# Optimization experiments

Measured on AMD Instinct MI355X. Metric: run time of the kernel, lower is better.

The kernel has to match this reference:

```python
import jax, jax.numpy as jnp
import numpy as np

B, S, E, H, MAXLEN = 2, 2048, 1024, 16, 2048


def _level_indices(seq_len: int, base: int = 2) -> np.ndarray:
    """Vectorized version of get_level_index_weak over the full (target, source) grid.
    indices[t, s] = min(level, 2) for s < t, else 0. Runs in O(log S) passes."""
    tt = np.broadcast_to(np.arange(seq_len)[:, None], (seq_len, seq_len)).astype(np.int64).copy()
    ss = np.broadcast_to(np.arange(seq_len)[None, :], (seq_len, seq_len)).astype(np.int64).copy()
    res = np.zeros((seq_len, seq_len), np.int64)
    done = ~(ss < tt)  # only source < target positions get a level; rest stay 0
    while not done.all():
        l = np.floor(np.log2(np.maximum(tt, 1).astype(np.float64))).astype(np.int64)
        v = (np.int64(1) << l)
        hit = (~done) & (ss < v)
        res[hit] = l[hit] + 1
        done |= hit
        step = ~done
        tt[step] -= v[step]
        ss[step] -= v[step]
    return np.minimum(res, 2).astype(np.int32)


def setup_inputs() -> dict:
    key = jax.random.key(0)
    ks = jax.random.split(key, 10)
    sc = 0.02
    return {
        "x": jax.random.normal(ks[0], (B, S, E), dtype=jnp.float32),
        "attention_mask": jax.random.randint(ks[1], (B, S), 0, 2, dtype=jnp.int32),
        "level_indices": jnp.asarray(_level_indices(S, 2)),
        "Wq": jax.random.normal(ks[2], (E, E), dtype=jnp.float32) * sc,
        "bq": jnp.zeros((E,), jnp.float32),
        "Wk": jax.random.normal(ks[3], (E, E), dtype=jnp.float32) * sc,
        "bk": jnp.zeros((E,), jnp.float32),
        "Wv": jax.random.normal(ks[4], (E, E), dtype=jnp.float32) * sc,
        "bv": jnp.zeros((E,), jnp.float32),
        "hier": jax.random.normal(ks[5], (MAXLEN, H, 3), dtype=jnp.float32),
        "Wo": jax.random.normal(ks[6], (E, E), dtype=jnp.float32) * sc,
        "bo": jnp.zeros((E,), jnp.float32),
    }


def reference(x, attention_mask, level_indices, Wq, bq, Wk, bk, Wv, bv, hier, Wo, bo):
    b, s, e = x.shape
    h = hier.shape[1]
    dh = e // h
    # q/k are computed by the original module but never used; kept for fidelity (zero grads).
    q = x @ Wq.T + bq
    k = x @ Wk.T + bk
    v = (x @ Wv.T + bv).reshape(b, s, h, dh).transpose(0, 2, 1, 3)  # [B,H,S,Dh]
    lev = level_indices[:s, :s]  # [S,S] int, values in {0,1,2}
    # Faithful torch.gather semantics: weights[b,h,i,j] = hier[b, h, lev[i,j]]
    w3 = hier[:b]                      # [B,H,3]
    weights = w3[:, :, lev]            # [B,H,S,S]
    decay = jnp.power(jnp.float32(0.5), lev.astype(x.dtype))  # [S,S]
    weights = weights * decay
    weights = weights / (jnp.sum(weights, axis=-1, keepdims=True) + 1e-8)
    weights = jnp.where(attention_mask[:, None, None, :] == 0, jnp.float32(0.0), weights)
    out = jnp.einsum('bhij,bhjd->bhid', weights, v)  # [B,H,S,Dh]
    out = out.transpose(0, 2, 1, 3).reshape(b, s, e)
    return out @ Wo.T + bo
```

## Files before the change

kernel.cpp:

```cpp
#include <hip/hip_runtime.h>
#include <cstdint>
#include <cstddef>

constexpr int Sn = 2048;
constexpr int En = 1024;
constexpr int Bn = 2;
constexpr int Hn = 16;
constexpr int NCH = 32;
constexpr int CHUNK = 64;

typedef __bf16 bf16x8 __attribute__((ext_vector_type(8)));
typedef float  f32x4  __attribute__((ext_vector_type(4)));

#define GLOBAL_AS(p) ((const __attribute__((address_space(1))) void*)(p))
#define LDS_AS(p)    ((__attribute__((address_space(3))) void*)(p))

__device__ __forceinline__ unsigned short f2bf(float f) {
    union { float f; uint32_t u; } v; v.f = f;
    const uint32_t u = v.u;
    return (unsigned short)((u + 0x7fffu + ((u >> 16) & 1u)) >> 16);
}
__device__ __forceinline__ float bf2f_lo(uint32_t u) {
    union { uint32_t u; float f; } v; v.u = u << 16; return v.f;
}
__device__ __forceinline__ float bf2f_hi(uint32_t u) {
    union { uint32_t u; float f; } v; v.u = u & 0xffff0000u; return v.f;
}

constexpr int XN = Bn * Sn * En;
constexpr int WN = En * En;

__global__ __launch_bounds__(256)
void cast3(const float* __restrict__ x, const float* __restrict__ Wv,
           const float* __restrict__ Wo, unsigned short* __restrict__ xb,
           unsigned short* __restrict__ Wvb, unsigned short* __restrict__ Wob)
{
    const int i = (blockIdx.x * 256 + threadIdx.x) * 4;
    const float* src; unsigned short* dst; int off;
    if (i < XN)           { src = x;  dst = xb;  off = i; }
    else if (i < XN + WN) { src = Wv; dst = Wvb; off = i - XN; }
    else                  { src = Wo; dst = Wob; off = i - XN - WN; }
    const float4 v = *(const float4*)(src + off);
    ushort4 o;
    o.x = f2bf(v.x); o.y = f2bf(v.y); o.z = f2bf(v.z); o.w = f2bf(v.w);
    *(ushort4*)(dst + off) = o;
}

template<bool APPLY_MASK, bool OUT_BF16, bool FUSE_CSUM>
__global__ __launch_bounds__(256)
void gemm_mfma(const unsigned short* __restrict__ A, const unsigned short* __restrict__ Bw,
               const float* __restrict__ bias, const int* __restrict__ mask,
               void* __restrict__ Cv, float* __restrict__ csum, int M, int N, int K)
{
    __shared__ __align__(16) unsigned short As[128 * 64];
    __shared__ __align__(16) unsigned short Bs[64 * 64];

    const int tid  = threadIdx.x;
    const int lane = tid & 63;
    const int wv   = tid >> 6;
    const int wr   = wv >> 1;
    const int wc   = wv & 1;
    const int bm   = blockIdx.y * 128;
    const int bn   = blockIdx.x * 64;
    const int m16  = lane & 15;
    const int kq   = lane >> 4;

    f32x4 acc[4][2] = {};

    const int j0 = 2 * wv, j1 = 2 * wv + 1;
    const unsigned short* gA0 = A  + (size_t)(bm + 16 * j0 + m16) * K + kq * 8;
    const unsigned short* gA1 = A  + (size_t)(bm + 16 * j1 + m16) * K + kq * 8;
    const unsigned short* gB0 = Bw + (size_t)(bn + 16 * wv + m16) * K + kq * 8;
    unsigned short* lA00 = &As[(j0 * 2 + 0) * 512];
    unsigned short* lA01 = &As[(j0 * 2 + 1) * 512];
    unsigned short* lA10 = &As[(j1 * 2 + 0) * 512];
    unsigned short* lA11 = &As[(j1 * 2 + 1) * 512];
    unsigned short* lB00 = &Bs[(wv * 2 + 0) * 512];
    unsigned short* lB01 = &Bs[(wv * 2 + 1) * 512];

    for (int k0 = 0; k0 < K; k0 += 64) {
        __syncthreads();
        __builtin_amdgcn_global_load_lds(GLOBAL_AS(gA0 + k0),      LDS_AS(lA00), 16, 0, 0);
        __builtin_amdgcn_global_load_lds(GLOBAL_AS(gA0 + k0 + 32), LDS_AS(lA01), 16, 0, 0);
        __builtin_amdgcn_global_load_lds(GLOBAL_AS(gA1 + k0),      LDS_AS(lA10), 16, 0, 0);
        __builtin_amdgcn_global_load_lds(GLOBAL_AS(gA1 + k0 + 32), LDS_AS(lA11), 16, 0, 0);
        __builtin_amdgcn_global_load_lds(GLOBAL_AS(gB0 + k0),      LDS_AS(lB00), 16, 0, 0);
        __builtin_amdgcn_global_load_lds(GLOBAL_AS(gB0 + k0 + 32), LDS_AS(lB01), 16, 0, 0);
        __syncthreads();

        bf16x8 af[4][2], bfr[2][2];
#pragma unroll
        for (int i = 0; i < 4; ++i)
#pragma unroll
            for (int kk = 0; kk < 2; ++kk)
                af[i][kk] = *(const bf16x8*)&As[((wr * 4 + i) * 2 + kk) * 512 + lane * 8];
#pragma unroll
        for (int j = 0; j < 2; ++j)
#pragma unroll
            for (int kk = 0; kk < 2; ++kk)
                bfr[j][kk] = *(const bf16x8*)&Bs[((wc * 2 + j) * 2 + kk) * 512 + lane * 8];
#pragma unroll
        for (int kk = 0; kk < 2; ++kk)
#pragma unroll
            for (int i = 0; i < 4; ++i)
#pragma unroll
                for (int j = 0; j < 2; ++j)
                    acc[i][j] = __builtin_amdgcn_mfma_f32_16x16x32_bf16(af[i][kk], bfr[j][kk], acc[i][j], 0, 0, 0);
    }

    float colsum[2] = {0.0f, 0.0f};
#pragma unroll
    for (int i = 0; i < 4; ++i) {
        const int r0 = bm + wr * 64 + i * 16 + kq * 4;
#pragma unroll
        for (int j = 0; j < 2; ++j) {
            const int c0 = bn + wc * 32 + j * 16 + m16;
            const float bcol = bias[c0];
#pragma unroll
            for (int r = 0; r < 4; ++r) {
                const int row = r0 + r;
                float val = acc[i][j][r] + bcol;
                if (APPLY_MASK) val = (mask[row] == 0) ? 0.0f : val;
                if (FUSE_CSUM) colsum[j] += val;
                if (OUT_BF16)
                    ((unsigned short*)Cv)[(size_t)row * N + c0] = f2bf(val);
                else
                    ((float*)Cv)[(size_t)row * N + c0] = val;
            }
        }
    }

    if (FUSE_CSUM) {
        const int gc = 2 * blockIdx.y + wr;
#pragma unroll
        for (int j = 0; j < 2; ++j) {
            float s = colsum[j];
            s += __shfl_xor(s, 16, 64);
            s += __shfl_xor(s, 32, 64);
            if (kq == 0)
                csum[(size_t)gc * En + bn + wc * 32 + j * 16 + m16] = s;
        }
    }
}

__global__ __launch_bounds__(256)
void chunk_scan(const float* __restrict__ csum, float* __restrict__ cscan,
                float* __restrict__ Tbuf)
{
    const int idx = blockIdx.x * 256 + threadIdx.x;
    float run = 0.0f;
    const int b = idx >> 10;
    const int e = idx & (En - 1);
    for (int c = 0; c < NCH; ++c) {
        const size_t off = ((size_t)b * NCH + c) * En + e;
        const float v = csum[off];
        cscan[off] = run;
        run += v;
    }
    Tbuf[idx] = run;
}

__global__ __launch_bounds__(256)
void combine(const unsigned short* __restrict__ vm, const float* __restrict__ cscan,
             const float* __restrict__ Tbuf, const float* __restrict__ hier,
             unsigned short* __restrict__ opre)
{
    const int ep = blockIdx.x * 256 + threadIdx.x;
    const int e = ep * 2;
    const int c = blockIdx.y;
    const int b = blockIdx.z;
    const int h = e >> 6;

    const float w0 = hier[((size_t)b * Hn + h) * 3 + 0];
    const float w1 = hier[((size_t)b * Hn + h) * 3 + 1] * 0.5f;
    const float w2 = hier[((size_t)b * Hn + h) * 3 + 2] * 0.25f;
    const float T0 = Tbuf[(size_t)b * En + e];
    const float T1 = Tbuf[(size_t)b * En + e + 1];

    const size_t co = ((size_t)b * NCH + c) * En + e;
    float run0 = cscan[co], run1 = cscan[co + 1];
    float prev0 = 0.0f, prev1 = 0.0f;
    const size_t base = ((size_t)b * Sn + c * CHUNK) * En + e;

    for (int t = 0; t < CHUNK; ++t) {
        const int i = c * CHUNK + t;
        const uint32_t u = *(const uint32_t*)(vm + base + (size_t)t * En);
        const float cur0 = bf2f_lo(u), cur1 = bf2f_hi(u);
        float num0, num1, Z;
        if (i & 1) {
            num0 = w2 * (run0 - prev0) + w1 * prev0 + w0 * (T0 - run0);
            num1 = w2 * (run1 - prev1) + w1 * prev1 + w0 * (T1 - run1);
            Z = (float)(i - 1) * w2 + w1 + (float)(Sn - i) * w0 + 1e-8f;
        } else {
            num0 = w2 * run0 + w0 * (T0 - run0);
            num1 = w2 * run1 + w0 * (T1 - run1);
            Z = (float)i * w2 + (float)(Sn - i) * w0 + 1e-8f;
        }
        const float rz = 1.0f / Z;
        const uint32_t o = (uint32_t)f2bf(num0 * rz) | ((uint32_t)f2bf(num1 * rz) << 16);
        *(uint32_t*)(opre + base + (size_t)t * En) = o;
        run0 += cur0; run1 += cur1;
        prev0 = cur0; prev1 = cur1;
    }
}

extern "C" void kernel_launch(void* const* d_in, const int* in_sizes, int n_in,
                              void* d_out, int out_size, void* d_ws, size_t ws_size,
                              hipStream_t stream)
{
    const float* x    = (const float*)d_in[0];
    const int*   mask = (const int*)d_in[1];
    const float* Wv   = (const float*)d_in[7];
    const float* bv   = (const float*)d_in[8];
    const float* hier = (const float*)d_in[9];
    const float* Wo   = (const float*)d_in[10];
    const float* bo   = (const float*)d_in[11];
    float* out = (float*)d_out;

    const int M = Bn * Sn, N = En, K = En;

    char* ws = (char*)d_ws;
    unsigned short* xb    = (unsigned short*)ws;  ws += (size_t)M * K * 2;
    unsigned short* Wvb   = (unsigned short*)ws;  ws += (size_t)N * K * 2;
    unsigned short* Wob   = (unsigned short*)ws;  ws += (size_t)N * K * 2;
    unsigned short* vmb   = (unsigned short*)ws;  ws += (size_t)M * N * 2;
    float*          csum  = (float*)ws;           ws += (size_t)Bn * NCH * En * 4;
    float*          cscan = (float*)ws;           ws += (size_t)Bn * NCH * En * 4;
    float*          Tbuf  = (float*)ws;           ws += (size_t)Bn * En * 4;
    unsigned short* opreb = (unsigned short*)ws;  ws += (size_t)M * N * 2;

    dim3 threads(256);

    cast3<<<dim3((XN + 2 * WN) / 1024), threads, 0, stream>>>(x, Wv, Wo, xb, Wvb, Wob);

    dim3 gemm_grid(N / 64, M / 128);

    gemm_mfma<true, true, true><<<gemm_grid, threads, 0, stream>>>(xb, Wvb, bv, mask, vmb, csum, M, N, K);
    chunk_scan<<<dim3((Bn * En) / 256), threads, 0, stream>>>(csum, cscan, Tbuf);
    combine<<<dim3(En / 512, NCH, Bn), threads, 0, stream>>>(vmb, cscan, Tbuf, hier, opreb);
    gemm_mfma<false, false, false><<<gemm_grid, threads, 0, stream>>>(opreb, Wob, bo, nullptr, out, nullptr, M, N, K);
}
```

Baseline: 172.3 us.

## Switch GEMMs to 128x128 split-K tiles with separate reduction kernels

Both GEMMs now use 128x128 output tiles with K split in two across blockIdx.z, writing fp32 partials to a workspace. New reduce kernels sum the partials and apply bias, mask, bf16 cast and per-chunk column sums. The chunk_scan kernel is dropped; combine recomputes the prefix and total from csum itself. This raises per-tile reuse and keeps the grid at 512 blocks, but it adds about 32 MB of fp32 partial traffic per GEMM plus two extra launches.

```diff
diff --git a/kernel.cpp b/kernel.cpp
--- a/kernel.cpp
+++ b/kernel.cpp
@@ -8,6 +8,8 @@
 constexpr int Hn = 16;
 constexpr int NCH = 32;
 constexpr int CHUNK = 64;
+constexpr int Mtot = Bn * Sn;
+constexpr int GCH = Mtot / CHUNK;
 
 typedef __bf16 bf16x8 __attribute__((ext_vector_type(8)));
 typedef float  f32x4  __attribute__((ext_vector_type(4)));
@@ -46,14 +48,12 @@
     *(ushort4*)(dst + off) = o;
 }
 
-template<bool APPLY_MASK, bool OUT_BF16, bool FUSE_CSUM>
-__global__ __launch_bounds__(256)
-void gemm_mfma(const unsigned short* __restrict__ A, const unsigned short* __restrict__ Bw,
-               const float* __restrict__ bias, const int* __restrict__ mask,
-               void* __restrict__ Cv, float* __restrict__ csum, int M, int N, int K)
+__global__ __launch_bounds__(256)
+void gemm_splitk(const unsigned short* __restrict__ A, const unsigned short* __restrict__ Bw,
+                 float* __restrict__ Part, int M, int N, int K)
 {
     __shared__ __align__(16) unsigned short As[128 * 64];
-    __shared__ __align__(16) unsigned short Bs[64 * 64];
+    __shared__ __align__(16) unsigned short Bs[128 * 64];
 
     const int tid  = threadIdx.x;
     const int lane = tid & 63;
@@ -61,24 +61,30 @@
     const int wr   = wv >> 1;
     const int wc   = wv & 1;
     const int bm   = blockIdx.y * 128;
-    const int bn   = blockIdx.x * 64;
+    const int bn   = blockIdx.x * 128;
+    const int ks   = blockIdx.z;
     const int m16  = lane & 15;
     const int kq   = lane >> 4;
 
-    f32x4 acc[4][2] = {};
-
-    const int j0 = 2 * wv, j1 = 2 * wv + 1;
-    const unsigned short* gA0 = A  + (size_t)(bm + 16 * j0 + m16) * K + kq * 8;
-    const unsigned short* gA1 = A  + (size_t)(bm + 16 * j1 + m16) * K + kq * 8;
-    const unsigned short* gB0 = Bw + (size_t)(bn + 16 * wv + m16) * K + kq * 8;
-    unsigned short* lA00 = &As[(j0 * 2 + 0) * 512];
-    unsigned short* lA01 = &As[(j0 * 2 + 1) * 512];
-    unsigned short* lA10 = &As[(j1 * 2 + 0) * 512];
-    unsigned short* lA11 = &As[(j1 * 2 + 1) * 512];
-    unsigned short* lB00 = &Bs[(wv * 2 + 0) * 512];
-    unsigned short* lB01 = &Bs[(wv * 2 + 1) * 512];
-
-    for (int k0 = 0; k0 < K; k0 += 64) {
+    const int kbase = ks * (K / 2);
+
+    f32x4 acc[4][4] = {};
+
+    const int rg0 = 2 * wv, rg1 = 2 * wv + 1;
+    const unsigned short* gA0 = A  + (size_t)(bm + 16 * rg0 + m16) * K + kbase + kq * 8;
+    const unsigned short* gA1 = A  + (size_t)(bm + 16 * rg1 + m16) * K + kbase + kq * 8;
+    const unsigned short* gB0 = Bw + (size_t)(bn + 16 * rg0 + m16) * K + kbase + kq * 8;
+    const unsigned short* gB1 = Bw + (size_t)(bn + 16 * rg1 + m16) * K + kbase + kq * 8;
+    unsigned short* lA00 = &As[(rg0 * 2 + 0) * 512];
+    unsigned short* lA01 = &As[(rg0 * 2 + 1) * 512];
+    unsigned short* lA10 = &As[(rg1 * 2 + 0) * 512];
+    unsigned short* lA11 = &As[(rg1 * 2 + 1) * 512];
+    unsigned short* lB00 = &Bs[(rg0 * 2 + 0) * 512];
+    unsigned short* lB01 = &Bs[(rg0 * 2 + 1) * 512];
+    unsigned short* lB10 = &Bs[(rg1 * 2 + 0) * 512];
+    unsigned short* lB11 = &Bs[(rg1 * 2 + 1) * 512];
+
+    for (int k0 = 0; k0 < K / 2; k0 += 64) {
         __syncthreads();
         __builtin_amdgcn_global_load_lds(GLOBAL_AS(gA0 + k0),      LDS_AS(lA00), 16, 0, 0);
         __builtin_amdgcn_global_load_lds(GLOBAL_AS(gA0 + k0 + 32), LDS_AS(lA01), 16, 0, 0);
@@ -86,84 +92,81 @@
         __builtin_amdgcn_global_load_lds(GLOBAL_AS(gA1 + k0 + 32), LDS_AS(lA11), 16, 0, 0);
         __builtin_amdgcn_global_load_lds(GLOBAL_AS(gB0 + k0),      LDS_AS(lB00), 16, 0, 0);
         __builtin_amdgcn_global_load_lds(GLOBAL_AS(gB0 + k0 + 32), LDS_AS(lB01), 16, 0, 0);
+        __builtin_amdgcn_global_load_lds(GLOBAL_AS(gB1 + k0),      LDS_AS(lB10), 16, 0, 0);
+        __builtin_amdgcn_global_load_lds(GLOBAL_AS(gB1 + k0 + 32), LDS_AS(lB11), 16, 0, 0);
         __syncthreads();
 
-        bf16x8 af[4][2], bfr[2][2];
+        bf16x8 af[4][2], bfr[4][2];
 #pragma unroll
         for (int i = 0; i < 4; ++i)
 #pragma unroll
-            for (int kk = 0; kk < 2; ++kk)
-                af[i][kk] = *(const bf16x8*)&As[((wr * 4 + i) * 2 + kk) * 512 + lane * 8];
-#pragma unroll
-        for (int j = 0; j < 2; ++j)
-#pragma unroll
-            for (int kk = 0; kk < 2; ++kk)
-                bfr[j][kk] = *(const bf16x8*)&Bs[((wc * 2 + j) * 2 + kk) * 512 + lane * 8];
-#pragma unroll
-        for (int kk = 0; kk < 2; ++kk)
+            for (int kh = 0; kh < 2; ++kh) {
+                af[i][kh]  = *(const bf16x8*)&As[(((wr * 4 + i) * 2) + kh) * 512 + lane * 8];
+                bfr[i][kh] = *(const bf16x8*)&Bs[(((wc * 4 + i) * 2) + kh) * 512 + lane * 8];
+            }
+#pragma unroll
+        for (int kh = 0; kh < 2; ++kh)
 #pragma unroll
             for (int i = 0; i < 4; ++i)
 #pragma unroll
-                for (int j = 0; j < 2; ++j)
-                    acc[i][j] = __builtin_amdgcn_mfma_f32_16x16x32_bf16(af[i][kk], bfr[j][kk], acc[i][j], 0, 0, 0);
-    }
-
-    float colsum[2] = {0.0f, 0.0f};
+                for (int j = 0; j < 4; ++j)
+                    acc[i][j] = __builtin_amdgcn_mfma_f32_16x16x32_bf16(af[i][kh], bfr[j][kh], acc[i][j], 0, 0, 0);
+    }
+
+    float* P = Part + (size_t)ks * M * N;
 #pragma unroll
     for (int i = 0; i < 4; ++i) {
         const int r0 = bm + wr * 64 + i * 16 + kq * 4;
 #pragma unroll
-        for (int j = 0; j < 2; ++j) {
-            const int c0 = bn + wc * 32 + j * 16 + m16;
-            const float bcol = bias[c0];
-#pragma unroll
-            for (int r = 0; r < 4; ++r) {
-                const int row = r0 + r;
-                float val = acc[i][j][r] + bcol;
-                if (APPLY_MASK) val = (mask[row] == 0) ? 0.0f : val;
-                if (FUSE_CSUM) colsum[j] += val;
-                if (OUT_BF16)
-                    ((unsigned short*)Cv)[(size_t)row * N + c0] = f2bf(val);
-                else
-                    ((float*)Cv)[(size_t)row * N + c0] = val;
-            }
+        for (int j = 0; j < 4; ++j) {
+            const int c0 = bn + wc * 64 + j * 16 + m16;
+#pragma unroll
+            for (int r = 0; r < 4; ++r)
+                P[(size_t)(r0 + r) * N + c0] = acc[i][j][r];
         }
     }
-
-    if (FUSE_CSUM) {
-        const int gc = 2 * blockIdx.y + wr;
-#pragma unroll
-        for (int j = 0; j < 2; ++j) {
-            float s = colsum[j];
-            s += __shfl_xor(s, 16, 64);
-            s += __shfl_xor(s, 32, 64);
-            if (kq == 0)
-                csum[(size_t)gc * En + bn + wc * 32 + j * 16 + m16] = s;
-        }
-    }
-}
-
-__global__ __launch_bounds__(256)
-void chunk_scan(const float* __restrict__ csum, float* __restrict__ cscan,
-                float* __restrict__ Tbuf)
-{
-    const int idx = blockIdx.x * 256 + threadIdx.x;
-    float run = 0.0f;
-    const int b = idx >> 10;
-    const int e = idx & (En - 1);
-    for (int c = 0; c < NCH; ++c) {
-        const size_t off = ((size_t)b * NCH + c) * En + e;
-        const float v = csum[off];
-        cscan[off] = run;
-        run += v;
-    }
-    Tbuf[idx] = run;
-}
-
-__global__ __launch_bounds__(256)
-void combine(const unsigned short* __restrict__ vm, const float* __restrict__ cscan,
-             const float* __restrict__ Tbuf, const float* __restrict__ hier,
-             unsigned short* __restrict__ opre)
+}
+
+__global__ __launch_bounds__(256)
+void reduce1(const float* __restrict__ Part, const float* __restrict__ bv,
+             const int* __restrict__ mask, unsigned short* __restrict__ vmb,
+             float* __restrict__ csum)
+{
+    const int e = blockIdx.x * 256 + threadIdx.x;
+    const int g = blockIdx.y;
+    const float bias = bv[e];
+    const float* P0 = Part;
+    const float* P1 = Part + (size_t)Mtot * En;
+    float s = 0.0f;
+    const int row0 = g * CHUNK;
+    for (int r = 0; r < CHUNK; ++r) {
+        const int row = row0 + r;
+        const size_t off = (size_t)row * En + e;
+        float v = P0[off] + P1[off] + bias;
+        v = (mask[row] == 0) ? 0.0f : v;
+        s += v;
+        vmb[off] = f2bf(v);
+    }
+    csum[(size_t)g * En + e] = s;
+}
+
+__global__ __launch_bounds__(256)
+void reduce2(const float* __restrict__ Part, const float* __restrict__ bo,
+             float* __restrict__ out)
+{
+    const size_t i = ((size_t)blockIdx.x * 256 + threadIdx.x) * 4;
+    const float4 p0 = *(const float4*)(Part + i);
+    const float4 p1 = *(const float4*)(Part + (size_t)Mtot * En + i);
+    const float4 bb = *(const float4*)(bo + (i & (En - 1)));
+    float4 o;
+    o.x = p0.x + p1.x + bb.x; o.y = p0.y + p1.y + bb.y;
+    o.z = p0.z + p1.z + bb.z; o.w = p0.w + p1.w + bb.w;
+    *(float4*)(out + i) = o;
+}
+
+__global__ __launch_bounds__(256)
+void combine(const unsigned short* __restrict__ vm, const float* __restrict__ csum,
+             const float* __restrict__ hier, unsigned short* __restrict__ opre)
 {
     const int ep = blockIdx.x * 256 + threadIdx.x;
     const int e = ep * 2;
@@ -174,11 +177,16 @@
     const float w0 = hier[((size_t)b * Hn + h) * 3 + 0];
     const float w1 = hier[((size_t)b * Hn + h) * 3 + 1] * 0.5f;
     const float w2 = hier[((size_t)b * Hn + h) * 3 + 2] * 0.25f;
-    const float T0 = Tbuf[(size_t)b * En + e];
-    const float T1 = Tbuf[(size_t)b * En + e + 1];
-
-    const size_t co = ((size_t)b * NCH + c) * En + e;
-    float run0 = cscan[co], run1 = cscan[co + 1];
+
+    float run0 = 0.0f, run1 = 0.0f, T0 = 0.0f, T1 = 0.0f;
+    const int g0 = b * NCH;
+    for (int c2 = 0; c2 < NCH; ++c2) {
+        const size_t off = (size_t)(g0 + c2) * En + e;
+        const float v0 = csum[off], v1 = csum[off + 1];
+        if (c2 < c) { run0 += v0; run1 += v1; }
+        T0 += v0; T1 += v1;
+    }
+
     float prev0 = 0.0f, prev1 = 0.0f;
     const size_t base = ((size_t)b * Sn + c * CHUNK) * En + e;
 
@@ -217,26 +225,26 @@
     const float* bo   = (const float*)d_in[11];
     float* out = (float*)d_out;
 
-    const int M = Bn * Sn, N = En, K = En;
+    const int M = Mtot, N = En, K = En;
 
     char* ws = (char*)d_ws;
     unsigned short* xb    = (unsigned short*)ws;  ws += (size_t)M * K * 2;
     unsigned short* Wvb   = (unsigned short*)ws;  ws += (size_t)N * K * 2;
     unsigned short* Wob   = (unsigned short*)ws;  ws += (size_t)N * K * 2;
     unsigned short* vmb   = (unsigned short*)ws;  ws += (size_t)M * N * 2;
-    float*          csum  = (float*)ws;           ws += (size_t)Bn * NCH * En * 4;
-    float*          cscan = (float*)ws;           ws += (size_t)Bn * NCH * En * 4;
-    float*          Tbuf  = (float*)ws;           ws += (size_t)Bn * En * 4;
+    float*          csum  = (float*)ws;           ws += (size_t)GCH * En * 4;
     unsigned short* opreb = (unsigned short*)ws;  ws += (size_t)M * N * 2;
+    float*          Part  = (float*)ws;           ws += (size_t)2 * M * N * 4;
 
     dim3 threads(256);
 
     cast3<<<dim3((XN + 2 * WN) / 1024), threads, 0, stream>>>(x, Wv, Wo, xb, Wvb, Wob);
 
-    dim3 gemm_grid(N / 64, M / 128);
-
-    gemm_mfma<true, true, true><<<gemm_grid, threads, 0, stream>>>(xb, Wvb, bv, mask, vmb, csum, M, N, K);
-    chunk_scan<<<dim3((Bn * En) / 256), threads, 0, stream>>>(csum, cscan, Tbuf);
-    combine<<<dim3(En / 512, NCH, Bn), threads, 0, stream>>>(vmb, cscan, Tbuf, hier, opreb);
-    gemm_mfma<false, false, false><<<gemm_grid, threads, 0, stream>>>(opreb, Wob, bo, nullptr, out, nullptr, M, N, K);
-}
+    dim3 gemm_grid(N / 128, M / 128, 2);
+
+    gemm_splitk<<<gemm_grid, threads, 0, stream>>>(xb, Wvb, Part, M, N, K);
+    reduce1<<<dim3(En / 256, GCH), threads, 0, stream>>>(Part, bv, mask, vmb, csum);
+    combine<<<dim3(En / 512, NCH, Bn), threads, 0, stream>>>(vmb, csum, hier, opreb);
+    gemm_splitk<<<gemm_grid, threads, 0, stream>>>(opreb, Wob, Part, M, N, K);
+    reduce2<<<dim3((M * N) / 1024), threads, 0, stream>>>(Part, bo, out);
+}
```

Measured after the change: 180.7 us. +4.9%, slower.

## Register-prefetch GEMM tiles and fold chunk scan into combine kernel

Applied to the files above, without the earlier changes.

The GEMM drops direct global-to-LDS loads and instead prefetches the next K tile into registers while the current tile is computed, then stores it to LDS (software double buffering through registers). The separate chunk_scan kernel is removed: each combine thread now reads all per-chunk column sums itself to build its prefix and total, which saves a launch and the intermediate buffers. In exchange the GEMM uses more registers and a hardcoded 8-iteration K loop that assumes K=1024, and combine does redundant csum reads.

```diff
diff --git a/kernel.cpp b/kernel.cpp
--- a/kernel.cpp
+++ b/kernel.cpp
@@ -8,12 +8,11 @@
 constexpr int Hn = 16;
 constexpr int NCH = 32;
 constexpr int CHUNK = 64;
+constexpr int Mtot = Bn * Sn;
+constexpr int GCH = Mtot / CHUNK;
 
 typedef __bf16 bf16x8 __attribute__((ext_vector_type(8)));
 typedef float  f32x4  __attribute__((ext_vector_type(4)));
-
-#define GLOBAL_AS(p) ((const __attribute__((address_space(1))) void*)(p))
-#define LDS_AS(p)    ((__attribute__((address_space(3))) void*)(p))
 
 __device__ __forceinline__ unsigned short f2bf(float f) {
     union { float f; uint32_t u; } v; v.f = f;
@@ -48,7 +47,7 @@
 
 template<bool APPLY_MASK, bool OUT_BF16, bool FUSE_CSUM>
 __global__ __launch_bounds__(256)
-void gemm_mfma(const unsigned short* __restrict__ A, const unsigned short* __restrict__ Bw,
+void gemm_pipe(const unsigned short* __restrict__ A, const unsigned short* __restrict__ Bw,
                const float* __restrict__ bias, const int* __restrict__ mask,
                void* __restrict__ Cv, float* __restrict__ csum, int M, int N, int K)
 {
@@ -67,45 +66,63 @@
 
     f32x4 acc[4][2] = {};
 
-    const int j0 = 2 * wv, j1 = 2 * wv + 1;
-    const unsigned short* gA0 = A  + (size_t)(bm + 16 * j0 + m16) * K + kq * 8;
-    const unsigned short* gA1 = A  + (size_t)(bm + 16 * j1 + m16) * K + kq * 8;
-    const unsigned short* gB0 = Bw + (size_t)(bn + 16 * wv + m16) * K + kq * 8;
-    unsigned short* lA00 = &As[(j0 * 2 + 0) * 512];
-    unsigned short* lA01 = &As[(j0 * 2 + 1) * 512];
-    unsigned short* lA10 = &As[(j1 * 2 + 0) * 512];
-    unsigned short* lA11 = &As[(j1 * 2 + 1) * 512];
-    unsigned short* lB00 = &Bs[(wv * 2 + 0) * 512];
-    unsigned short* lB01 = &Bs[(wv * 2 + 1) * 512];
-
-    for (int k0 = 0; k0 < K; k0 += 64) {
-        __syncthreads();
-        __builtin_amdgcn_global_load_lds(GLOBAL_AS(gA0 + k0),      LDS_AS(lA00), 16, 0, 0);
-        __builtin_amdgcn_global_load_lds(GLOBAL_AS(gA0 + k0 + 32), LDS_AS(lA01), 16, 0, 0);
-        __builtin_amdgcn_global_load_lds(GLOBAL_AS(gA1 + k0),      LDS_AS(lA10), 16, 0, 0);
-        __builtin_amdgcn_global_load_lds(GLOBAL_AS(gA1 + k0 + 32), LDS_AS(lA11), 16, 0, 0);
-        __builtin_amdgcn_global_load_lds(GLOBAL_AS(gB0 + k0),      LDS_AS(lB00), 16, 0, 0);
-        __builtin_amdgcn_global_load_lds(GLOBAL_AS(gB0 + k0 + 32), LDS_AS(lB01), 16, 0, 0);
-        __syncthreads();
-
+    const int rg0 = 2 * wv, rg1 = 2 * wv + 1;
+    const unsigned short* gA0 = A  + (size_t)(bm + 16 * rg0 + m16) * K + kq * 8;
+    const unsigned short* gA1 = A  + (size_t)(bm + 16 * rg1 + m16) * K + kq * 8;
+    const unsigned short* gB0 = Bw + (size_t)(bn + 16 * wv  + m16) * K + kq * 8;
+    uint4* lA00 = (uint4*)&As[(rg0 * 2 + 0) * 512 + lane * 8];
+    uint4* lA01 = (uint4*)&As[(rg0 * 2 + 1) * 512 + lane * 8];
+    uint4* lA10 = (uint4*)&As[(rg1 * 2 + 0) * 512 + lane * 8];
+    uint4* lA11 = (uint4*)&As[(rg1 * 2 + 1) * 512 + lane * 8];
+    uint4* lB00 = (uint4*)&Bs[(wv  * 2 + 0) * 512 + lane * 8];
+    uint4* lB01 = (uint4*)&Bs[(wv  * 2 + 1) * 512 + lane * 8];
+
+    auto load6 = [&](uint4 r[6], int k0) {
+        r[0] = *(const uint4*)(gA0 + k0); r[1] = *(const uint4*)(gA0 + k0 + 32);
+        r[2] = *(const uint4*)(gA1 + k0); r[3] = *(const uint4*)(gA1 + k0 + 32);
+        r[4] = *(const uint4*)(gB0 + k0); r[5] = *(const uint4*)(gB0 + k0 + 32);
+    };
+    auto store6 = [&](const uint4 r[6]) {
+        *lA00 = r[0]; *lA01 = r[1];
+        *lA10 = r[2]; *lA11 = r[3];
+        *lB00 = r[4]; *lB01 = r[5];
+    };
+    auto compute = [&]() {
         bf16x8 af[4][2], bfr[2][2];
 #pragma unroll
         for (int i = 0; i < 4; ++i)
 #pragma unroll
-            for (int kk = 0; kk < 2; ++kk)
-                af[i][kk] = *(const bf16x8*)&As[((wr * 4 + i) * 2 + kk) * 512 + lane * 8];
+            for (int kh = 0; kh < 2; ++kh)
+                af[i][kh] = *(const bf16x8*)&As[((wr * 4 + i) * 2 + kh) * 512 + lane * 8];
 #pragma unroll
         for (int j = 0; j < 2; ++j)
 #pragma unroll
-            for (int kk = 0; kk < 2; ++kk)
-                bfr[j][kk] = *(const bf16x8*)&Bs[((wc * 2 + j) * 2 + kk) * 512 + lane * 8];
-#pragma unroll
-        for (int kk = 0; kk < 2; ++kk)
+            for (int kh = 0; kh < 2; ++kh)
+                bfr[j][kh] = *(const bf16x8*)&Bs[((wc * 2 + j) * 2 + kh) * 512 + lane * 8];
+#pragma unroll
+        for (int kh = 0; kh < 2; ++kh)
 #pragma unroll
             for (int i = 0; i < 4; ++i)
 #pragma unroll
                 for (int j = 0; j < 2; ++j)
-                    acc[i][j] = __builtin_amdgcn_mfma_f32_16x16x32_bf16(af[i][kk], bfr[j][kk], acc[i][j], 0, 0, 0);
+                    acc[i][j] = __builtin_amdgcn_mfma_f32_16x16x32_bf16(af[i][kh], bfr[j][kh], acc[i][j], 0, 0, 0);
+    };
+
+    uint4 rA[6], rB[6];
+    load6(rA, 0);
+    for (int it = 0; it < 8; ++it) {
+        const int kbase = it * 128;
+        __syncthreads();
+        store6(rA);
+        __syncthreads();
+        load6(rB, kbase + 64);
+        compute();
+
+        __syncthreads();
+        store6(rB);
+        __syncthreads();
+        if (it < 7) load6(rA, kbase + 128);
+        compute();
     }
 
     float colsum[2] = {0.0f, 0.0f};
@@ -144,26 +161,8 @@
 }
 
 __global__ __launch_bounds__(256)
-void chunk_scan(const float* __restrict__ csum, float* __restrict__ cscan,
-                float* __restrict__ Tbuf)
-{
-    const int idx = blockIdx.x * 256 + threadIdx.x;
-    float run = 0.0f;
-    const int b = idx >> 10;
-    const int e = idx & (En - 1);
-    for (int c = 0; c < NCH; ++c) {
-        const size_t off = ((size_t)b * NCH + c) * En + e;
-        const float v = csum[off];
-        cscan[off] = run;
-        run += v;
-    }
-    Tbuf[idx] = run;
-}
-
-__global__ __launch_bounds__(256)
-void combine(const unsigned short* __restrict__ vm, const float* __restrict__ cscan,
-             const float* __restrict__ Tbuf, const float* __restrict__ hier,
-             unsigned short* __restrict__ opre)
+void combine(const unsigned short* __restrict__ vm, const float* __restrict__ csum,
+             const float* __restrict__ hier, unsigned short* __restrict__ opre)
 {
     const int ep = blockIdx.x * 256 + threadIdx.x;
     const int e = ep * 2;
@@ -174,11 +173,16 @@
     const float w0 = hier[((size_t)b * Hn + h) * 3 + 0];
     const float w1 = hier[((size_t)b * Hn + h) * 3 + 1] * 0.5f;
     const float w2 = hier[((size_t)b * Hn + h) * 3 + 2] * 0.25f;
-    const float T0 = Tbuf[(size_t)b * En + e];
-    const float T1 = Tbuf[(size_t)b * En + e + 1];
-
-    const size_t co = ((size_t)b * NCH + c) * En + e;
-    float run0 = cscan[co], run1 = cscan[co + 1];
+
+    float run0 = 0.0f, run1 = 0.0f, T0 = 0.0f, T1 = 0.0f;
+    const int g0 = b * NCH;
+    for (int c2 = 0; c2 < NCH; ++c2) {
+        const size_t off = (size_t)(g0 + c2) * En + e;
+        const float v0 = csum[off], v1 = csum[off + 1];
+        if (c2 < c) { run0 += v0; run1 += v1; }
+        T0 += v0; T1 += v1;
+    }
+
     float prev0 = 0.0f, prev1 = 0.0f;
     const size_t base = ((size_t)b * Sn + c * CHUNK) * En + e;
 
@@ -217,16 +221,14 @@
     const float* bo   = (const float*)d_in[11];
     float* out = (float*)d_out;
 
-    const int M = Bn * Sn, N = En, K = En;
+    const int M = Mtot, N = En, K = En;
 
     char* ws = (char*)d_ws;
     unsigned short* xb    = (unsigned short*)ws;  ws += (size_t)M * K * 2;
     unsigned short* Wvb   = (unsigned short*)ws;  ws += (size_t)N * K * 2;
     unsigned short* Wob   = (unsigned short*)ws;  ws += (size_t)N * K * 2;
     unsigned short* vmb   = (unsigned short*)ws;  ws += (size_t)M * N * 2;
-    float*          csum  = (float*)ws;           ws += (size_t)Bn * NCH * En * 4;
-    float*          cscan = (float*)ws;           ws += (size_t)Bn * NCH * En * 4;
-    float*          Tbuf  = (float*)ws;           ws += (size_t)Bn * En * 4;
+    float*          csum  = (float*)ws;           ws += (size_t)GCH * En * 4;
     unsigned short* opreb = (unsigned short*)ws;  ws += (size_t)M * N * 2;
 
     dim3 threads(256);
@@ -235,8 +237,7 @@
 
     dim3 gemm_grid(N / 64, M / 128);
 
-    gemm_mfma<true, true, true><<<gemm_grid, threads, 0, stream>>>(xb, Wvb, bv, mask, vmb, csum, M, N, K);
-    chunk_scan<<<dim3((Bn * En) / 256), threads, 0, stream>>>(csum, cscan, Tbuf);
-    combine<<<dim3(En / 512, NCH, Bn), threads, 0, stream>>>(vmb, cscan, Tbuf, hier, opreb);
-    gemm_mfma<false, false, false><<<gemm_grid, threads, 0, stream>>>(opreb, Wob, bo, nullptr, out, nullptr, M, N, K);
-}
+    gemm_pipe<true, true, true><<<gemm_grid, threads, 0, stream>>>(xb, Wvb, bv, mask, vmb, csum, M, N, K);
+    combine<<<dim3(En / 512, NCH, Bn), threads, 0, stream>>>(vmb, csum, hier, opreb);
+    gemm_pipe<false, false, false><<<gemm_grid, threads, 0, stream>>>(opreb, Wob, bo, nullptr, out, nullptr, M, N, K);
+}
```

After: 256.0 us. 1.49x slower.
